# Optimization experiments

Measured on AMD Instinct MI355X. Metric: run time of the kernel, lower is better.

Reference implementation:

```python
import jax, jax.numpy as jnp
import numpy as np

STEP, LEAK = 16, 32
KS = STEP + LEAK          # kernel_size = 48
FODEP = KS                # forced depression window
SYNAPSES, NEURONS = 64, 256
IC, OC = 1, 10
DENSE = 0.5
THETA = DENSE * SYNAPSES * IC   # 32.0
BIAS = 0.5
BATCH, TIME = 16, 512


def setup_inputs() -> dict:
    key = jax.random.key(0)
    k1, k2 = jax.random.split(key)
    # binary input spikes, density 0.2
    input_spikes = (jax.random.uniform(k1, (BATCH, IC, SYNAPSES, TIME)) < 0.2).astype(jnp.float32)
    # weight ~ Exponential(rate=1/w_init=2).sample().clip(0,1), mean 0.5
    u = jax.random.uniform(k2, (OC * NEURONS, IC * SYNAPSES), minval=1e-6, maxval=1.0)
    weight = jnp.clip(-0.5 * jnp.log(u), 0.0, 1.0)
    return {"input_spikes": input_spikes, "weight": weight}


def _step_fire_leak_kernel(weight):
    # kernel[o, i, t] = max(0, min(t/step, -(t - w*step)/leak + w)), flipped on t
    t = jnp.arange(KS, dtype=weight.dtype)
    t_spike = t / STEP                                        # rising edge
    t_leak = -(t - weight[..., None] * STEP) / LEAK + weight[..., None]  # decaying edge
    kernel = jnp.maximum(jnp.zeros((), weight.dtype), jnp.minimum(t_spike, t_leak))
    return kernel[..., ::-1]


def _forward(input_spikes, weight):
    B, C, S, T = input_spikes.shape
    x = input_spikes.reshape(B, C * S, T)
    kernel = _step_fire_leak_kernel(weight)                   # [OC*N, IC*S, KS]
    # conv1d with padding = kernel_size on both sides -> T' = T + KS + 1
    pot = jax.lax.conv_general_dilated(
        x, kernel, window_strides=(1,), padding=[(KS, KS)],
        dimension_numbers=("NCH", "OIH", "NCH"))
    Tp = pot.shape[-1]
    pot = pot.reshape(B, OC, NEURONS, Tp) + BIAS * THETA      # unsupervised bias path

    # winner-takes-all scan over time with per-(batch, neuron) depression counter
    pot_t = pot.transpose(3, 0, 2, 1)                         # [T', B, N, OC]
    dep0 = jnp.zeros((B, NEURONS, OC), jnp.int32)

    def step_fn(dep, p):
        masked = jnp.where(dep == 0, p, jnp.zeros((), p.dtype))
        winner = jnp.argmax(masked, axis=-1)                  # [B, N]
        wpot = jnp.take_along_axis(masked, winner[..., None], axis=-1)[..., 0]
        spike = (wpot > THETA).astype(p.dtype)                # [B, N]
        w_t = jax.nn.one_hot(winner, OC, dtype=p.dtype) * spike[..., None]
        dep = jnp.clip(dep + spike.astype(jnp.int32)[..., None] * FODEP - 1, 0, FODEP - 1)
        return dep, w_t

    _, winners = jax.lax.scan(step_fn, dep0, pot_t)           # [T', B, N, OC]
    return winners.transpose(1, 3, 2, 0)                      # [B, OC, N, T'] float


def reference(input_spikes, weight):
    return _forward(input_spikes, weight)
```

## Files before the change

kernel.cpp:

```cpp
#include <hip/hip_runtime.h>

#define B_   16
#define OC_  10
#define N_   256
#define O_   2560
#define S_   64
#define T_   512
#define KS_  48
#define TP_  561
#define TT   24
#define WROW 72

#define NOC   160
#define XROWS 624
#define JC    12
#define NPH   (KS_/JC)

#define SCH    16
#define CPITCH 572

using i32x4 = __attribute__((ext_vector_type(4))) int;

__global__ void prep_all(const float* __restrict__ x, const float* __restrict__ w,
                         unsigned char* __restrict__ xb, signed char* __restrict__ Bg) {
    if (blockIdx.x < 2048) {
        int idx = blockIdx.x * 256 + threadIdx.x;
        int t = idx & 511;
        int bi = idx >> 9;
        int i = bi & 63, b = bi >> 6;
        xb[((size_t)(b * 512 + t) << 6) + i] = (x[idx] != 0.0f) ? 1 : 0;
    } else {
        int idx = (blockIdx.x - 2048) * 256 + threadIdx.x;
        int i = idx & 63;
        int oj = idx >> 6;
        int j = oj % KS_, o = oj / KS_;
        float wv = w[(o << 6) + i];
        float rise = (float)j * 0.0625f;
        float leak = -((float)j - wv * 16.0f) * 0.03125f + wv;
        float kv   = fmaxf(0.0f, fminf(rise, leak));
        int q  = (int)lrintf(kv * 4194304.0f);
        int d0 = ((q + 128) & 255) - 128;
        int q1 = (q - d0) >> 8;
        int d1 = ((q1 + 128) & 255) - 128;
        int d2 = (q1 - d1) >> 8;
        int oc = o >> 4, ol = o & 15;
        int jm = j & 15, jh = j >> 4;
        int pos = (jm >> 2) * 12 + (jm & 3) * 3 + jh;
        int key = (ol >> 1) & 3;
        int bpos = ((((i >> 4) ^ key) << 4) | (i & 15));
        size_t base = (((size_t)(oc * KS_ + pos) * 48) + ol) * 64 + bpos;
        Bg[base]            = (signed char)d0;
        Bg[base + 16 * 64]  = (signed char)d1;
        Bg[base + 32 * 64]  = (signed char)d2;
    }
}

__global__ __launch_bounds__(256, 2) void gemm_i8(
    const unsigned char* __restrict__ xb,
    const signed char*  __restrict__ Bg,
    float* __restrict__ pot)
{
    __shared__ __align__(16) unsigned char xT[XROWS * 64];
    __shared__ __align__(16) signed char  Bst[JC * 48 * 64];

    const int tid  = threadIdx.x;
    const int lane = tid & 63;
    const int wave = tid >> 6;
    const int oc = blockIdx.x;
    const int b  = blockIdx.y;
    const int lrow = lane & 15;
    const int quad = lane >> 4;
    const int tw = wave * 144;
    const int coffB = ((quad ^ ((lrow >> 1) & 3)) << 4);

    const signed char* BgBase = Bg + (size_t)oc * KS_ * 48 * 64;

    auto stage = [&](int ph) {
        const signed char* src = BgBase + (size_t)(ph * JC) * 48 * 64;
        for (int c = tid; c < JC * 48 * 64 / 16; c += 256)
            __builtin_amdgcn_global_load_lds(
                (const __attribute__((address_space(1))) void*)(src + c * 16),
                (__attribute__((address_space(3))) void*)(Bst + c * 16),
                16, 0, 0);
    };

    stage(0);

    for (int z = tid; z < 112 * 4; z += 256) {
        int zi = z >> 2, p = z & 3;
        int r = (zi < 49) ? zi : (561 + zi - 49);
        *(i32x4*)(xT + r * 64 + p * 16) = (i32x4){0, 0, 0, 0};
    }
    const unsigned char* xbb = xb + ((size_t)b << 15);
    for (int q = tid; q < 2048; q += 256) {
        i32x4 v = *(const i32x4*)(xbb + q * 16);
        int t = q >> 2, p = q & 3;
        int r = 49 + t;
        *(i32x4*)(xT + r * 64 + ((p ^ ((r >> 1) & 3)) << 4)) = v;
    }

    i32x4 acc[9][3];
#pragma unroll
    for (int mi = 0; mi < 9; ++mi)
#pragma unroll
        for (int f = 0; f < 3; ++f)
            acc[mi][f] = (i32x4){0, 0, 0, 0};

    __syncthreads();

    for (int ph = 0; ph < NPH; ++ph) {
#pragma unroll
        for (int tloc = 0; tloc < 4; ++tloc) {
            const int j0 = ph * 4 + tloc;
            const int rb = tw + 16 - j0 + lrow;
            const int coffA = ((quad ^ ((rb >> 1) & 3)) << 4);
            i32x4 af[11], bf[3][3];
#pragma unroll
            for (int k = 0; k < 11; ++k)
                af[k] = *(const i32x4*)(xT + (rb + k * 16) * 64 + coffA);
#pragma unroll
            for (int jh = 0; jh < 3; ++jh)
#pragma unroll
                for (int f = 0; f < 3; ++f)
                    bf[jh][f] = *(const i32x4*)
                        (Bst + (((tloc * 3 + jh) * 48) + f * 16 + lrow) * 64 + coffB);
#pragma unroll
            for (int jh = 0; jh < 3; ++jh)
#pragma unroll
                for (int mi = 0; mi < 9; ++mi)
#pragma unroll
                    for (int f = 0; f < 3; ++f)
                        acc[mi][f] = __builtin_amdgcn_mfma_i32_16x16x64_i8(
                            af[mi + 2 - jh], bf[jh][f], acc[mi][f], 0, 0, 0);
        }
        __syncthreads();
        if (ph + 1 < NPH) {
            stage(ph + 1);
            __syncthreads();
        }
    }

    const size_t potb = (size_t)b * TP_;
#pragma unroll
    for (int mi = 0; mi < 9; ++mi) {
#pragma unroll
        for (int r = 0; r < 4; ++r) {
            int t = tw + mi * 16 + quad * 4 + r;
            if (t < TP_) {
                double pq = ((double)acc[mi][0][r]
                           + 256.0   * (double)acc[mi][1][r]
                           + 65536.0 * (double)acc[mi][2][r])
                          * (1.0 / 4194304.0);
                pot[(potb + t) * O_ + oc * 16 + lrow] = (float)pq;
            }
        }
    }
}

__global__ __launch_bounds__(1024) void scan_fused(
    const float* __restrict__ pot,
    float* __restrict__ out)
{
    __shared__ unsigned char codeW[SCH * CPITCH];
    __shared__ unsigned char ocW[SCH * CPITCH];

    const int tid = threadIdx.x;
    const int nc = blockIdx.x;
    const int b  = blockIdx.y;
    const int n0 = nc * SCH;

    for (int pair = tid; pair < TP_ * SCH; pair += 1024) {
        int t = pair >> 4, nl = pair & 15;
        const float* p = pot + ((size_t)(b * TP_ + t)) * O_ + n0 + nl;
        float best = p[0]; int bo = 0;
#pragma unroll
        for (int ch = 1; ch < OC_; ++ch) {
            float v = p[ch * N_];
            if (v > best) { best = v; bo = ch; }
        }
        codeW[nl * CPITCH + t] =
            ((best + 16.0f) > 32.0f) ? (unsigned char)(bo + 1) : (unsigned char)0;
        ocW[nl * CPITCH + t] = 0;
    }
    __syncthreads();

    if (tid < SCH) {
        const unsigned char* c = &codeW[tid * CPITCH];
        unsigned char* o = &ocW[tid * CPITCH];
        int t = 0;
        while (t < TP_) {
            unsigned char buf[KS_];
#pragma unroll
            for (int k = 0; k < KS_; ++k) {
                int tt = t + k;
                buf[k] = (tt < TP_) ? c[tt] : (unsigned char)0;
            }
            int adv = KS_;
#pragma unroll
            for (int k = 0; k < KS_; ++k) {
                if (buf[k]) { o[t + k] = buf[k]; adv = k + KS_; break; }
            }
            t += adv;
        }
    }
    __syncthreads();

    float* ob = out + (((size_t)b * OC_) * N_ + n0) * TP_;
    for (int idx = tid; idx < OC_ * SCH * TP_; idx += 1024) {
        int r = idx / TP_;
        int t = idx - r * TP_;
        int ch = r >> 4, nl = r & 15;
        float v = (ocW[nl * CPITCH + t] == (unsigned char)(ch + 1)) ? 1.0f : 0.0f;
        ob[((size_t)ch * N_ + nl) * TP_ + t] = v;
    }
}

__global__ void transpose_w(const float* __restrict__ w, float* __restrict__ wT) {
    int idx = blockIdx.x * 256 + threadIdx.x;
    if (idx >= O_ * S_) return;
    int o = idx >> 6, i = idx & 63;
    wT[i * O_ + o] = w[idx];
}

__global__ __launch_bounds__(256) void conv_kernel(
    const float* __restrict__ x, const float* __restrict__ wT,
    float* __restrict__ pot)
{
    const int b  = blockIdx.y;
    const int t0 = blockIdx.z * TT;
    const int o  = blockIdx.x * 256 + threadIdx.x;

    __shared__ __align__(16) float xsh[S_][WROW];
    for (int idx = threadIdx.x; idx < S_ * WROW; idx += 256) {
        int i = idx / WROW, m = idx - i * WROW;
        int t = t0 - KS_ + m;
        float v = 0.0f;
        if (t >= 0 && t < T_) v = x[(b * S_ + i) * T_ + t];
        xsh[i][m] = v;
    }
    __syncthreads();

    float acch[TT], accl[TT];
#pragma unroll
    for (int tl = 0; tl < TT; ++tl) { acch[tl] = 0.0f; accl[tl] = 0.0f; }

    for (int i = 0; i < S_; ++i) {
        float xw[WROW];
#pragma unroll
        for (int w4 = 0; w4 < WROW / 4; ++w4) {
            const float4 v = *reinterpret_cast<const float4*>(&xsh[i][w4 * 4]);
            xw[w4 * 4 + 0] = v.x; xw[w4 * 4 + 1] = v.y;
            xw[w4 * 4 + 2] = v.z; xw[w4 * 4 + 3] = v.w;
        }
        const float wv = wT[i * O_ + o];
#pragma unroll
        for (int j = 1; j < KS_; ++j) {
            float rise = (float)j * 0.0625f;
            float leak = -((float)j - wv * 16.0f) * 0.03125f + wv;
            float kv   = fmaxf(0.0f, fminf(rise, leak));
            float khi  = rintf(kv * 4096.0f) * 2.44140625e-4f;
            float klo  = kv - khi;
#pragma unroll
            for (int tl = 0; tl < TT; ++tl) {
                float xv = xw[tl + (KS_ - 1) - j];
                acch[tl] = fmaf(xv, khi, acch[tl]);
                accl[tl] = fmaf(xv, klo, accl[tl]);
            }
        }
    }
#pragma unroll
    for (int tl = 0; tl < TT; ++tl) {
        int t = t0 + tl;
        if (t < TP_) pot[((size_t)b * TP_ + t) * O_ + o] = acch[tl] + accl[tl];
    }
}

__global__ void scan_prep(const float* __restrict__ pot, unsigned char* __restrict__ code) {
    int idx = blockIdx.x * 256 + threadIdx.x;
    if (idx >= B_ * TP_ * N_) return;
    int n  = idx & (N_ - 1);
    int bt = idx >> 8;
    const float* p = pot + (size_t)bt * O_ + n;
    float best = p[0]; int bo = 0;
#pragma unroll
    for (int oc = 1; oc < OC_; ++oc) {
        float v = p[oc * N_];
        if (v > best) { best = v; bo = oc; }
    }
    code[idx] = ((best + 16.0f) > 32.0f) ? (unsigned char)(bo + 1) : (unsigned char)0;
}

__global__ void scan_run(const unsigned char* __restrict__ code, float* __restrict__ out) {
    int idx = blockIdx.x * 256 + threadIdx.x;
    if (idx >= B_ * N_) return;
    int b = idx >> 8, n = idx & 255;
    const unsigned char* c = code + (size_t)b * TP_ * N_ + n;
    int t = 0;
    while (t < TP_) {
        unsigned char buf[KS_];
#pragma unroll
        for (int k = 0; k < KS_; ++k) {
            int tt = t + k;
            buf[k] = (tt < TP_) ? c[(size_t)tt * N_] : (unsigned char)0;
        }
        int adv = KS_;
#pragma unroll
        for (int k = 0; k < KS_; ++k) {
            if (buf[k]) {
                out[(((size_t)b * OC_ + (buf[k] - 1)) * N_ + n) * TP_ + (t + k)] = 1.0f;
                adv = k + KS_;
                break;
            }
        }
        t += adv;
    }
}

extern "C" void kernel_launch(void* const* d_in, const int* in_sizes, int n_in,
                              void* d_out, int out_size, void* d_ws, size_t ws_size,
                              hipStream_t stream) {
    const float* x = (const float*)d_in[0];
    const float* w = (const float*)d_in[1];
    float* out = (float*)d_out;

    char* ws = (char*)d_ws;
    const size_t szX = (size_t)B_ * T_ * S_;
    const size_t szB = (size_t)NOC * KS_ * 48 * 64;
    const size_t szP = (size_t)B_ * TP_ * O_ * 4;
    const size_t szC = (size_t)B_ * TP_ * N_;
    const size_t need = szX + szB + szP + szC;

    if (ws_size >= need) {
        unsigned char* xb  = (unsigned char*)ws;
        signed char* Bg    = (signed char*)(ws + szX);
        float* pot         = (float*)(ws + szX + szB);

        prep_all<<<2048 + 30720, 256, 0, stream>>>(x, w, xb, Bg);
        gemm_i8<<<dim3(NOC, B_), 256, 0, stream>>>(xb, Bg, pot);
        scan_fused<<<dim3(N_ / SCH, B_), 1024, 0, stream>>>(pot, out);
    } else {
        size_t pot_bytes  = (size_t)B_ * TP_ * O_ * sizeof(float);
        size_t code_bytes = (size_t)B_ * TP_ * N_;
        float* pot = (float*)ws;
        unsigned char* code = (unsigned char*)(ws + pot_bytes);
        float* wT = (float*)(ws + pot_bytes + code_bytes);

        hipMemsetAsync(d_out, 0, (size_t)out_size * sizeof(float), stream);
        transpose_w<<<(O_ * S_ + 255) / 256, 256, 0, stream>>>(w, wT);
        conv_kernel<<<dim3(O_ / 256, B_, (TP_ + TT - 1) / TT), 256, 0, stream>>>(x, wT, pot);
        scan_prep<<<(B_ * TP_ * N_ + 255) / 256, 256, 0, stream>>>(pot, code);
        scan_run<<<(B_ * N_ + 255) / 256, 256, 0, stream>>>(code, out);
    }
}
```

Baseline: 269.8 us.

## Switch int8 conv GEMM to 32x32x32 MFMA tiles with time-split blocks

Reworks the int8 implicit-GEMM convolution to use 32x32x32 i8 MFMA instructions on 32-output-channel tiles instead of 16x16x64 on 16-channel tiles. The grid gains a z dimension that splits the time axis into two halves, with 3 waves per block each covering 96 time rows. The weight pre-layout and LDS staging are rebuilt to match: 96 rows per tap and 6 taps per phase. This is meant to raise MFMA efficiency and cut the redundant A-fragment LDS reads per tap. In exchange, the split recomputes the overlapping halo rows, and with 3 waves per block the occupancy and tail behaviour change.

```diff
diff --git a/kernel.cpp b/kernel.cpp
--- a/kernel.cpp
+++ b/kernel.cpp
@@ -11,15 +11,16 @@
 #define TT   24
 #define WROW 72
 
-#define NOC   160
-#define XROWS 624
-#define JC    12
-#define NPH   (KS_/JC)
+#define NOC32  80
+#define XLROWS 336
+#define JC     6
+#define NPH    (KS_/JC)
 
 #define SCH    16
 #define CPITCH 572
 
-using i32x4 = __attribute__((ext_vector_type(4))) int;
+using i32x4  = __attribute__((ext_vector_type(4))) int;
+using i32x16 = __attribute__((ext_vector_type(16))) int;
 
 __global__ void prep_all(const float* __restrict__ x, const float* __restrict__ w,
                          unsigned char* __restrict__ xb, signed char* __restrict__ Bg) {
@@ -43,41 +44,39 @@
         int q1 = (q - d0) >> 8;
         int d1 = ((q1 + 128) & 255) - 128;
         int d2 = (q1 - d1) >> 8;
-        int oc = o >> 4, ol = o & 15;
-        int jm = j & 15, jh = j >> 4;
-        int pos = (jm >> 2) * 12 + (jm & 3) * 3 + jh;
+        int oc = o >> 5, ol = o & 31;
         int key = (ol >> 1) & 3;
         int bpos = ((((i >> 4) ^ key) << 4) | (i & 15));
-        size_t base = (((size_t)(oc * KS_ + pos) * 48) + ol) * 64 + bpos;
+        size_t base = (((size_t)(oc * KS_ + j) * 96) + ol) * 64 + bpos;
         Bg[base]            = (signed char)d0;
-        Bg[base + 16 * 64]  = (signed char)d1;
-        Bg[base + 32 * 64]  = (signed char)d2;
-    }
-}
-
-__global__ __launch_bounds__(256, 2) void gemm_i8(
+        Bg[base + 32 * 64]  = (signed char)d1;
+        Bg[base + 64 * 64]  = (signed char)d2;
+    }
+}
+
+__global__ __launch_bounds__(192, 2) void gemm_i8(
     const unsigned char* __restrict__ xb,
     const signed char*  __restrict__ Bg,
     float* __restrict__ pot)
 {
-    __shared__ __align__(16) unsigned char xT[XROWS * 64];
-    __shared__ __align__(16) signed char  Bst[JC * 48 * 64];
+    __shared__ __align__(16) unsigned char xT[XLROWS * 64];
+    __shared__ __align__(16) signed char  Bst[JC * 96 * 64];
 
     const int tid  = threadIdx.x;
     const int lane = tid & 63;
     const int wave = tid >> 6;
     const int oc = blockIdx.x;
     const int b  = blockIdx.y;
-    const int lrow = lane & 15;
-    const int quad = lane >> 4;
-    const int tw = wave * 144;
-    const int coffB = ((quad ^ ((lrow >> 1) & 3)) << 4);
-
-    const signed char* BgBase = Bg + (size_t)oc * KS_ * 48 * 64;
+    const int mh = blockIdx.z;
+    const int l31 = lane & 31;
+    const int lh  = lane >> 5;
+    const int keyB = (l31 >> 1) & 3;
+
+    const signed char* BgBase = Bg + (size_t)oc * (KS_ * 96 * 64);
 
     auto stage = [&](int ph) {
-        const signed char* src = BgBase + (size_t)(ph * JC) * 48 * 64;
-        for (int c = tid; c < JC * 48 * 64 / 16; c += 256)
+        const signed char* src = BgBase + (size_t)(ph * JC) * 96 * 64;
+        for (int c = tid; c < JC * 96 * 64 / 16; c += 192)
             __builtin_amdgcn_global_load_lds(
                 (const __attribute__((address_space(1))) void*)(src + c * 16),
                 (__attribute__((address_space(3))) void*)(Bst + c * 16),
@@ -86,52 +85,54 @@
 
     stage(0);
 
-    for (int z = tid; z < 112 * 4; z += 256) {
-        int zi = z >> 2, p = z & 3;
-        int r = (zi < 49) ? zi : (561 + zi - 49);
-        *(i32x4*)(xT + r * 64 + p * 16) = (i32x4){0, 0, 0, 0};
-    }
     const unsigned char* xbb = xb + ((size_t)b << 15);
-    for (int q = tid; q < 2048; q += 256) {
-        i32x4 v = *(const i32x4*)(xbb + q * 16);
-        int t = q >> 2, p = q & 3;
-        int r = 49 + t;
-        *(i32x4*)(xT + r * 64 + ((p ^ ((r >> 1) & 3)) << 4)) = v;
-    }
-
-    i32x4 acc[9][3];
-#pragma unroll
-    for (int mi = 0; mi < 9; ++mi)
-#pragma unroll
-        for (int f = 0; f < 3; ++f)
-            acc[mi][f] = (i32x4){0, 0, 0, 0};
+    for (int c = tid; c < XLROWS * 4; c += 192) {
+        int rl = c >> 2, p = c & 3;
+        int r = mh * 288 + rl;
+        i32x4 v = (i32x4){0, 0, 0, 0};
+        if (r >= 49 && r <= 560) v = *(const i32x4*)(xbb + (size_t)(r - 49) * 64 + p * 16);
+        *(i32x4*)(xT + rl * 64 + ((p ^ ((rl >> 1) & 3)) << 4)) = v;
+    }
+
+    i32x16 acc[3][3];
+#pragma unroll
+    for (int mt = 0; mt < 3; ++mt)
+#pragma unroll
+        for (int d = 0; d < 3; ++d)
+#pragma unroll
+            for (int r = 0; r < 16; ++r)
+                acc[mt][d][r] = 0;
 
     __syncthreads();
 
     for (int ph = 0; ph < NPH; ++ph) {
 #pragma unroll
-        for (int tloc = 0; tloc < 4; ++tloc) {
-            const int j0 = ph * 4 + tloc;
-            const int rb = tw + 16 - j0 + lrow;
-            const int coffA = ((quad ^ ((rb >> 1) & 3)) << 4);
-            i32x4 af[11], bf[3][3];
-#pragma unroll
-            for (int k = 0; k < 11; ++k)
-                af[k] = *(const i32x4*)(xT + (rb + k * 16) * 64 + coffA);
-#pragma unroll
-            for (int jh = 0; jh < 3; ++jh)
-#pragma unroll
-                for (int f = 0; f < 3; ++f)
-                    bf[jh][f] = *(const i32x4*)
-                        (Bst + (((tloc * 3 + jh) * 48) + f * 16 + lrow) * 64 + coffB);
-#pragma unroll
-            for (int jh = 0; jh < 3; ++jh)
-#pragma unroll
-                for (int mi = 0; mi < 9; ++mi)
-#pragma unroll
-                    for (int f = 0; f < 3; ++f)
-                        acc[mi][f] = __builtin_amdgcn_mfma_i32_16x16x64_i8(
-                            af[mi + 2 - jh], bf[jh][f], acc[mi][f], 0, 0, 0);
+        for (int jl = 0; jl < JC; ++jl) {
+            const int j = ph * JC + jl;
+            const int rbase = wave * 96 + l31 + 48 - j;
+            const int keyA = (rbase >> 1) & 3;
+            i32x4 af[3][2], bf[3][2];
+#pragma unroll
+            for (int mt = 0; mt < 3; ++mt)
+#pragma unroll
+                for (int kc = 0; kc < 2; ++kc)
+                    af[mt][kc] = *(const i32x4*)
+                        (xT + (rbase + mt * 32) * 64 + (((kc * 2 + lh) ^ keyA) << 4));
+#pragma unroll
+            for (int d = 0; d < 3; ++d)
+#pragma unroll
+                for (int kc = 0; kc < 2; ++kc)
+                    bf[d][kc] = *(const i32x4*)
+                        (Bst + (size_t)(jl * 96 + d * 32 + l31) * 64
+                             + (((kc * 2 + lh) ^ keyB) << 4));
+#pragma unroll
+            for (int mt = 0; mt < 3; ++mt)
+#pragma unroll
+                for (int d = 0; d < 3; ++d)
+#pragma unroll
+                    for (int kc = 0; kc < 2; ++kc)
+                        acc[mt][d] = __builtin_amdgcn_mfma_i32_32x32x32_i8(
+                            af[mt][kc], bf[d][kc], acc[mt][d], 0, 0, 0);
         }
         __syncthreads();
         if (ph + 1 < NPH) {
@@ -141,17 +142,19 @@
     }
 
     const size_t potb = (size_t)b * TP_;
-#pragma unroll
-    for (int mi = 0; mi < 9; ++mi) {
-#pragma unroll
-        for (int r = 0; r < 4; ++r) {
-            int t = tw + mi * 16 + quad * 4 + r;
+    const int oo = oc * 32 + l31;
+#pragma unroll
+    for (int mt = 0; mt < 3; ++mt) {
+#pragma unroll
+        for (int reg = 0; reg < 16; ++reg) {
+            int t = mh * 288 + wave * 96 + mt * 32
+                  + (reg & 3) + 8 * (reg >> 2) + 4 * lh;
             if (t < TP_) {
-                double pq = ((double)acc[mi][0][r]
-                           + 256.0   * (double)acc[mi][1][r]
-                           + 65536.0 * (double)acc[mi][2][r])
+                double pq = ((double)acc[mt][0][reg]
+                           + 256.0   * (double)acc[mt][1][reg]
+                           + 65536.0 * (double)acc[mt][2][reg])
                           * (1.0 / 4194304.0);
-                pot[(potb + t) * O_ + oc * 16 + lrow] = (float)pq;
+                pot[(potb + t) * O_ + oo] = (float)pq;
             }
         }
     }
@@ -325,7 +328,7 @@
 
     char* ws = (char*)d_ws;
     const size_t szX = (size_t)B_ * T_ * S_;
-    const size_t szB = (size_t)NOC * KS_ * 48 * 64;
+    const size_t szB = (size_t)NOC32 * KS_ * 96 * 64;
     const size_t szP = (size_t)B_ * TP_ * O_ * 4;
     const size_t szC = (size_t)B_ * TP_ * N_;
     const size_t need = szX + szB + szP + szC;
@@ -336,7 +339,7 @@
         float* pot         = (float*)(ws + szX + szB);
 
         prep_all<<<2048 + 30720, 256, 0, stream>>>(x, w, xb, Bg);
-        gemm_i8<<<dim3(NOC, B_), 256, 0, stream>>>(xb, Bg, pot);
+        gemm_i8<<<dim3(NOC32, B_, 2), 192, 0, stream>>>(xb, Bg, pot);
         scan_fused<<<dim3(N_ / SCH, B_), 1024, 0, stream>>>(pot, out);
     } else {
         size_t pot_bytes  = (size_t)B_ * TP_ * O_ * sizeof(float);
```

New measurement: 325.3 us. +20.6%, slower.
